# Kernel optimization log

Hardware: AMD Instinct MI355X
Metric: run time of the kernel (lower is better)

The kernel has to match this reference:

```python
import jax, jax.numpy as jnp
import numpy as np

N = 50000      # nodes
E = 500000     # edges
CHAN = 64      # channels
R0 = 2.0       # radial cutoff scale


def radial_encode_8(d, r0):
    # d: (E,) edge distances -> (E, 8) Gaussian radial basis on [0, r0]
    mu = jnp.linspace(0.0, r0, 8).astype(d.dtype)
    sigma = r0 / 8.0
    return jnp.exp(-(((d[:, None] - mu) / sigma) ** 2))


def vector_sigmoid(v):
    # v: (..., 3, chan); sigmoid-shaped vector activation (norm over spatial axis)
    vv = jnp.sum(v * v, axis=-2, keepdims=True)
    return v / jnp.sqrt(1.0 + vv)


def setup_inputs() -> dict:
    key = jax.random.key(0)
    ks = jax.random.split(key, 12)
    rn = lambda i, shape, scale=1.0: jax.random.normal(ks[i], shape, jnp.float32) * scale
    src = jax.random.randint(ks[0], (E,), 0, N)
    dst = jax.random.randint(ks[1], (E,), 0, N)
    r_ij = rn(2, (E, 3))
    z_0 = rn(3, (N, CHAN))
    z_1 = rn(4, (N, 3, CHAN))
    emb = rn(5, (N, CHAN))
    k = CHAN ** -0.5
    return dict(
        src=src, dst=dst, r_ij=r_ij, z_0=z_0, z_1=z_1, emb=emb,
        W_enc=rn(6, (8, CHAN), 8 ** -0.5), b_enc=jnp.zeros((CHAN,), jnp.float32),
        W_src=rn(7, (CHAN, CHAN), k), b_src=jnp.zeros((CHAN,), jnp.float32),
        W_dst=rn(8, (CHAN, CHAN), k), b_dst=jnp.zeros((CHAN,), jnp.float32),
        W_gate=rn(9, (CHAN, 4 * CHAN), k), b_gate=jnp.zeros((4 * CHAN,), jnp.float32),
        W_s=rn(10, (CHAN, CHAN), k), W_v=rn(11, (CHAN, CHAN), k),
    )


def reference(src, dst, r_ij, z_0, z_1, emb,
              W_enc, b_enc, W_src, b_src, W_dst, b_dst,
              W_gate, b_gate, W_s, W_v):
    # edges_read: gather node embeddings to edges, fuse src/dst linears
    emb_ij = (emb[src] @ W_src + b_src) + (emb[dst] @ W_dst + b_dst)        # (E, C)
    d = jnp.sqrt(jnp.sum(r_ij * r_ij, axis=-1))                              # (E,)
    dist_emb = radial_encode_8(d, R0) @ W_enc + b_enc + emb_ij               # (E, C)
    # vector sigmoid on scaled displacement
    r_hat = vector_sigmoid((r_ij * (7.0 / R0))[..., None])[..., 0]           # (E, 3)
    # edges_read_dst: gather dst-node scalar/vector features
    z0_j = z_0[dst]                                                          # (E, C)
    z1_j = z_1[dst]                                                          # (E, 3, C)
    # MessageContract (rank-1 equivariant tensor contraction, gated by dist_emb)
    g = (dist_emb @ W_gate + b_gate).reshape(E, 4, CHAN)                     # (E, 4, C)
    s_msg = g[:, 0] * z0_j + g[:, 1] * jnp.einsum('ei,eic->ec', r_hat, z1_j)  # scalar msg
    psi0 = s_msg @ W_s                                                        # (E, C)
    v_msg = g[:, 2][:, None, :] * z1_j \
          + g[:, 3][:, None, :] * (r_hat[:, :, None] * z0_j[:, None, :])     # (E, 3, C)
    psi1 = jnp.einsum('eic,cd->eid', v_msg, W_v)                              # (E, 3, C)
    # edges_reduce_src: scatter-add messages back to source nodes
    out0 = jax.ops.segment_sum(psi0, src, num_segments=N)                     # (N, C)
    out1 = jax.ops.segment_sum(psi1.reshape(E, 3 * CHAN), src,
                               num_segments=N).reshape(N, 3, CHAN)            # (N, 3, C)
    return out0, out1
```

## Files before the change

### kernel.cpp

```cpp
#include <hip/hip_runtime.h>

typedef unsigned int u32;

#define WS_WSG   0
#define WS_WDG   16384
#define WS_WEG   32768
#define WS_BALL  34816
#define WS_GS    35072

__global__ void zero_k(float* p, int n) {
    int i = blockIdx.x * blockDim.x + threadIdx.x;
    int st = gridDim.x * blockDim.x;
    for (; i < n; i += st) p[i] = 0.0f;
}

__global__ void compose_k(const float* __restrict__ Wsrc, const float* __restrict__ Wdst,
                          const float* __restrict__ Wenc, const float* __restrict__ benc,
                          const float* __restrict__ bsrc, const float* __restrict__ bdst,
                          const float* __restrict__ Wgate, const float* __restrict__ bgate,
                          float* __restrict__ ws) {
    const int j = threadIdx.x;
    const int r = blockIdx.x;
    if (r < 64) {
        float a = 0.f, b = 0.f;
        for (int c = 0; c < 64; ++c) {
            const float wg = Wgate[c * 256 + j];
            a += Wsrc[r * 64 + c] * wg;
            b += Wdst[r * 64 + c] * wg;
        }
        ws[WS_WSG + r * 256 + j] = a;
        ws[WS_WDG + r * 256 + j] = b;
    } else if (r < 72) {
        const int m = r - 64;
        float a = 0.f;
        for (int c = 0; c < 64; ++c) a += Wenc[m * 64 + c] * Wgate[c * 256 + j];
        ws[WS_WEG + m * 256 + j] = a;
    } else {
        float a = bgate[j];
        for (int c = 0; c < 64; ++c)
            a += (benc[c] + bsrc[c] + bdst[c]) * Wgate[c * 256 + j];
        ws[WS_BALL + j] = a;
    }
}

__global__ __launch_bounds__(512, 1) void nodepre_k(
    const float* __restrict__ emb, const float* __restrict__ ws,
    float* __restrict__ GS, float* __restrict__ GD, int N) {
    __shared__ float sW[32768];
    __shared__ float sE[256];
    for (int i = threadIdx.x; i < 32768; i += 512) sW[i] = ws[i];
    __syncthreads();
    const int half = threadIdx.x >> 8;
    const int j = threadIdx.x & 255;
    const float* W = &sW[half * 16384];
    float* G = half ? GD : GS;
    const int ngroups = (N + 3) >> 2;
    for (int grp = blockIdx.x; grp < ngroups; grp += gridDim.x) {
        const int n0 = grp * 4;
        if (threadIdx.x < 256) {
            const int nn = n0 + (threadIdx.x >> 6);
            sE[threadIdx.x] = (nn < N) ? emb[nn * 64 + (threadIdx.x & 63)] : 0.f;
        }
        __syncthreads();
        float a0 = 0.f, a1 = 0.f, a2 = 0.f, a3 = 0.f;
        #pragma unroll 8
        for (int k = 0; k < 64; ++k) {
            const float w = W[k * 256 + j];
            a0 += sE[k] * w;
            a1 += sE[64 + k] * w;
            a2 += sE[128 + k] * w;
            a3 += sE[192 + k] * w;
        }
        if (n0 < N)     G[(size_t)n0 * 256 + j] = a0;
        if (n0 + 1 < N) G[(size_t)(n0 + 1) * 256 + j] = a1;
        if (n0 + 2 < N) G[(size_t)(n0 + 2) * 256 + j] = a2;
        if (n0 + 3 < N) G[(size_t)(n0 + 3) * 256 + j] = a3;
        __syncthreads();
    }
}

__global__ __launch_bounds__(256, 8) void edge_fast_k(
    const int* __restrict__ src, const int* __restrict__ dst,
    const float* __restrict__ r_ij, const float* __restrict__ z0g,
    const float* __restrict__ z1g, const float* __restrict__ GS,
    const float* __restrict__ GD, const float* __restrict__ WeG,
    const float* __restrict__ ball, float* __restrict__ out, int N, int E) {
    __shared__ float sWe[2048];
    __shared__ float sBall[256];
    __shared__ int sFl[2];

    if (threadIdx.x == 0) {
        const u32* ps = (const u32*)src;
        const u32* pd = (const u32*)dst;
        int s64 = 1, d64 = 1;
        for (int i = 1; i < 128; i += 2) {
            if (ps[i] != 0u) s64 = 0;
            if (pd[i] != 0u) d64 = 0;
        }
        sFl[0] = s64;
        sFl[1] = d64;
    }
    for (int i = threadIdx.x; i < 2048; i += 256) sWe[i] = WeG[i];
    if (threadIdx.x < 256) sBall[threadIdx.x] = ball[threadIdx.x];
    __syncthreads();

    const int wid = threadIdx.x >> 6, lane = threadIdx.x & 63;
    const int i64s = sFl[0], i64d = sFl[1];

    for (int e = blockIdx.x * 4 + wid; e < E; e += gridDim.x * 4) {
        const int s = i64s ? src[2 * e] : src[e];
        const int t = i64d ? dst[2 * e] : dst[e];
        if (s < 0 || s >= N || t < 0 || t >= N) continue;

        const float* gs = GS + (size_t)s * 256 + lane;
        const float* gd = GD + (size_t)t * 256 + lane;
        const float a0 = gs[0], a1 = gs[64], a2 = gs[128], a3 = gs[192];
        const float b0 = gd[0], b1 = gd[64], b2 = gd[128], b3 = gd[192];
        const float z0v = z0g[t * 64 + lane];
        const float za = z1g[t * 192 + lane];
        const float zb = z1g[t * 192 + 64 + lane];
        const float zc = z1g[t * 192 + 128 + lane];
        const float r0 = r_ij[e * 3 + 0];
        const float r1 = r_ij[e * 3 + 1];
        const float r2 = r_ij[e * 3 + 2];

        float g0 = a0 + b0 + sBall[lane];
        float g1 = a1 + b1 + sBall[64 + lane];
        float g2 = a2 + b2 + sBall[128 + lane];
        float g3 = a3 + b3 + sBall[192 + lane];

        const float d = sqrtf(r0 * r0 + r1 * r1 + r2 * r2);
        #pragma unroll
        for (int m = 0; m < 8; ++m) {
            const float mu = 0.28571428571f * (float)m;
            const float tt = (d - mu) * 4.0f;
            const float rm = __expf(-tt * tt);
            const float* w = &sWe[(m << 8) + lane];
            g0 += rm * w[0];
            g1 += rm * w[64];
            g2 += rm * w[128];
            g3 += rm * w[192];
        }

        const float v0 = r0 * 3.5f, v1 = r1 * 3.5f, v2 = r2 * 3.5f;
        const float inv = rsqrtf(1.0f + v0 * v0 + v1 * v1 + v2 * v2);
        const float h0 = v0 * inv, h1 = v1 * inv, h2 = v2 * inv;

        const float uu = h0 * za + h1 * zb + h2 * zc;

        const float smsg = g0 * z0v + g1 * uu;
        const float vm0 = g2 * za + g3 * h0 * z0v;
        const float vm1 = g2 * zb + g3 * h1 * z0v;
        const float vm2 = g2 * zc + g3 * h2 * z0v;

        atomicAdd(&out[s * 64 + lane], smsg);
        const int bo = N * 64 + s * 192 + lane;
        atomicAdd(&out[bo], vm0);
        atomicAdd(&out[bo + 64], vm1);
        atomicAdd(&out[bo + 128], vm2);
    }
}

__global__ __launch_bounds__(256) void nodepost_k(
    float* __restrict__ out, const float* __restrict__ Ws,
    const float* __restrict__ Wv, int N) {
    __shared__ float sWs[4096];
    __shared__ float sWv[4096];
    __shared__ float sRow[256];
    for (int i = threadIdx.x; i < 4096; i += 256) {
        sWs[i] = Ws[i];
        sWv[i] = Wv[i];
    }
    __syncthreads();
    const int j = threadIdx.x;
    const int part = j >> 6;
    const int col = j & 63;
    const float* W = (part == 0) ? sWs : sWv;
    for (int n = blockIdx.x; n < N; n += gridDim.x) {
        const float v = (part == 0) ? out[n * 64 + j]
                                    : out[N * 64 + n * 192 + (j - 64)];
        sRow[j] = v;
        __syncthreads();
        const float* row = &sRow[part * 64];
        float acc = 0.f;
        #pragma unroll 8
        for (int k = 0; k < 64; ++k) acc += row[k] * W[k * 64 + col];
        if (part == 0) out[n * 64 + j] = acc;
        else out[N * 64 + n * 192 + (j - 64)] = acc;
        __syncthreads();
    }
}

__global__ __launch_bounds__(512, 1) void edge_k(
    const int* __restrict__ src, const int* __restrict__ dst,
    const float* __restrict__ r_ij, const float* __restrict__ z0g,
    const float* __restrict__ z1g, const float* __restrict__ emb,
    const float* __restrict__ Wenc, const float* __restrict__ benc,
    const float* __restrict__ Wsrc, const float* __restrict__ bsrc,
    const float* __restrict__ Wdst, const float* __restrict__ bdst,
    const float* __restrict__ Wgate, const float* __restrict__ bgate,
    const float* __restrict__ Ws, const float* __restrict__ Wv,
    float* __restrict__ out, int N, int E)
{
    __shared__ float sWsrc[4096];
    __shared__ float sWdst[4096];
    __shared__ float sWg[16384];
    __shared__ float sWs[4096];
    __shared__ float sWv[4096];
    __shared__ float sWe[512];
    __shared__ float sB[64];
    __shared__ float sBg[256];
    __shared__ int sFl[2];

    if (threadIdx.x == 0) {
        const u32* ps = (const u32*)src;
        const u32* pd = (const u32*)dst;
        int s64 = 1, d64 = 1;
        for (int i = 1; i < 128; i += 2) {
            if (ps[i] != 0u) s64 = 0;
            if (pd[i] != 0u) d64 = 0;
        }
        sFl[0] = s64;
        sFl[1] = d64;
    }
    for (int i = threadIdx.x; i < 4096; i += 512) {
        sWsrc[i] = Wsrc[i];
        sWdst[i] = Wdst[i];
        sWs[i] = Ws[i];
        sWv[i] = Wv[i];
    }
    for (int i = threadIdx.x; i < 16384; i += 512) sWg[i] = Wgate[i];
    for (int i = threadIdx.x; i < 512; i += 512) sWe[i] = Wenc[i];
    if (threadIdx.x < 64)
        sB[threadIdx.x] = benc[threadIdx.x] + bsrc[threadIdx.x] + bdst[threadIdx.x];
    if (threadIdx.x < 256) sBg[threadIdx.x] = bgate[threadIdx.x];
    __syncthreads();

    const int wid = threadIdx.x >> 6, lane = threadIdx.x & 63;
    const int i64s = sFl[0], i64d = sFl[1];

    for (int e = blockIdx.x * 8 + wid; e < E; e += gridDim.x * 8) {
        const int s = i64s ? src[2 * e] : src[e];
        const int t = i64d ? dst[2 * e] : dst[e];
        if (s < 0 || s >= N || t < 0 || t >= N) continue;

        const float es = emb[s * 64 + lane];
        const float et = emb[t * 64 + lane];
        float de = sB[lane];
        #pragma unroll 8
        for (int k = 0; k < 64; ++k) {
            de += __shfl(es, k, 64) * sWsrc[(k << 6) + lane];
            de += __shfl(et, k, 64) * sWdst[(k << 6) + lane];
        }
        const float r0 = r_ij[e * 3 + 0];
        const float r1 = r_ij[e * 3 + 1];
        const float r2 = r_ij[e * 3 + 2];
        const float d = sqrtf(r0 * r0 + r1 * r1 + r2 * r2);
        #pragma unroll
        for (int m = 0; m < 8; ++m) {
            const float mu = (2.0f / 7.0f) * (float)m;
            const float tt = (d - mu) * 4.0f;
            de += __expf(-tt * tt) * sWe[m * 64 + lane];
        }

        const float v0 = r0 * 3.5f, v1 = r1 * 3.5f, v2 = r2 * 3.5f;
        const float inv = rsqrtf(1.0f + v0 * v0 + v1 * v1 + v2 * v2);
        const float h0 = v0 * inv, h1 = v1 * inv, h2 = v2 * inv;

        const float z0v = z0g[t * 64 + lane];
        const float za = z1g[t * 192 + lane];
        const float zb = z1g[t * 192 + 64 + lane];
        const float zc = z1g[t * 192 + 128 + lane];
        const float uu = h0 * za + h1 * zb + h2 * zc;

        float g0 = sBg[lane], g1 = sBg[64 + lane], g2 = sBg[128 + lane], g3 = sBg[192 + lane];
        #pragma unroll 8
        for (int k = 0; k < 64; ++k) {
            const float dk = __shfl(de, k, 64);
            const float* w = &sWg[(k << 8) + lane];
            g0 += dk * w[0];
            g1 += dk * w[64];
            g2 += dk * w[128];
            g3 += dk * w[192];
        }

        const float smsg = g0 * z0v + g1 * uu;
        const float vm0 = g2 * za + g3 * h0 * z0v;
        const float vm1 = g2 * zb + g3 * h1 * z0v;
        const float vm2 = g2 * zc + g3 * h2 * z0v;

        float p0 = 0.f, q0 = 0.f, q1 = 0.f, q2 = 0.f;
        #pragma unroll 8
        for (int k = 0; k < 64; ++k) {
            const float sk = __shfl(smsg, k, 64);
            const float a = __shfl(vm0, k, 64);
            const float b = __shfl(vm1, k, 64);
            const float c = __shfl(vm2, k, 64);
            p0 += sk * sWs[(k << 6) + lane];
            const float wv = sWv[(k << 6) + lane];
            q0 += a * wv;
            q1 += b * wv;
            q2 += c * wv;
        }

        atomicAdd(&out[s * 64 + lane], p0);
        const int b1 = N * 64 + s * 192 + lane;
        atomicAdd(&out[b1], q0);
        atomicAdd(&out[b1 + 64], q1);
        atomicAdd(&out[b1 + 128], q2);
    }
}

extern "C" void kernel_launch(void* const* d_in, const int* in_sizes, int n_in,
                              void* d_out, int out_size, void* d_ws, size_t ws_size,
                              hipStream_t stream) {
    const int* src = (const int*)d_in[0];
    const int* dst = (const int*)d_in[1];
    const float* r_ij = (const float*)d_in[2];
    const float* z0g  = (const float*)d_in[3];
    const float* z1g  = (const float*)d_in[4];
    const float* emb  = (const float*)d_in[5];
    const float* Wenc = (const float*)d_in[6];
    const float* benc = (const float*)d_in[7];
    const float* Wsrc = (const float*)d_in[8];
    const float* bsrc = (const float*)d_in[9];
    const float* Wdst = (const float*)d_in[10];
    const float* bdst = (const float*)d_in[11];
    const float* Wgate = (const float*)d_in[12];
    const float* bgate = (const float*)d_in[13];
    const float* Ws = (const float*)d_in[14];
    const float* Wv = (const float*)d_in[15];

    const int N = out_size / 256;
    int E = in_sizes[0];
    if (in_sizes[2] / 3 < E) E = in_sizes[2] / 3;

    zero_k<<<2048, 256, 0, stream>>>((float*)d_out, out_size);

    float* ws = (float*)d_ws;
    const size_t need = ((size_t)WS_GS + 2u * (size_t)N * 256u) * sizeof(float);
    if (ws != nullptr && ws_size >= need) {
        compose_k<<<73, 256, 0, stream>>>(Wsrc, Wdst, Wenc, benc, bsrc, bdst,
                                          Wgate, bgate, ws);
        float* GS = ws + WS_GS;
        float* GD = GS + (size_t)N * 256;
        nodepre_k<<<512, 512, 0, stream>>>(emb, ws, GS, GD, N);
        edge_fast_k<<<2048, 256, 0, stream>>>(src, dst, r_ij, z0g, z1g, GS, GD,
                                              ws + WS_WEG, ws + WS_BALL,
                                              (float*)d_out, N, E);
        nodepost_k<<<2048, 256, 0, stream>>>((float*)d_out, Ws, Wv, N);
    } else {
        edge_k<<<2048, 512, 0, stream>>>(src, dst, r_ij, z0g, z1g, emb, Wenc, benc,
                                         Wsrc, bsrc, Wdst, bdst, Wgate, bgate, Ws, Wv,
                                         (float*)d_out, N, E);
    }
}
```

Measured before the change: 789.7 us.

## Bucket edges by source node into CSR and accumulate messages per segment

Adds a counting sort of edges by source node (count, single-block scan, fill) that packs r_ij and dst into a float4 table. A new edge kernel walks contiguous source-sorted ranges, loads the source gate row once per segment and flushes register accumulators with one set of atomics per segment instead of per edge. The node pre- and post-transform kernels are also reworked with float4 shared reads and two rows per block. The sort adds several extra launches, a serial one-block scan and extra global traffic, and the sorted path only runs when the workspace is large enough.

```diff
diff --git a/kernel.cpp b/kernel.cpp
--- a/kernel.cpp
+++ b/kernel.cpp
@@ -6,7 +6,8 @@
 #define WS_WDG   16384
 #define WS_WEG   32768
 #define WS_BALL  34816
-#define WS_GS    35072
+#define WS_ETOT  35072
+#define WS_GS    35328
 
 __global__ void zero_k(float* p, int n) {
     int i = blockIdx.x * blockDim.x + threadIdx.x;
@@ -43,40 +44,215 @@
     }
 }
 
-__global__ __launch_bounds__(512, 1) void nodepre_k(
-    const float* __restrict__ emb, const float* __restrict__ ws,
-    float* __restrict__ GS, float* __restrict__ GD, int N) {
-    __shared__ float sW[32768];
-    __shared__ float sE[256];
-    for (int i = threadIdx.x; i < 32768; i += 512) sW[i] = ws[i];
-    __syncthreads();
-    const int half = threadIdx.x >> 8;
-    const int j = threadIdx.x & 255;
-    const float* W = &sW[half * 16384];
-    float* G = half ? GD : GS;
-    const int ngroups = (N + 3) >> 2;
-    for (int grp = blockIdx.x; grp < ngroups; grp += gridDim.x) {
-        const int n0 = grp * 4;
-        if (threadIdx.x < 256) {
-            const int nn = n0 + (threadIdx.x >> 6);
-            sE[threadIdx.x] = (nn < N) ? emb[nn * 64 + (threadIdx.x & 63)] : 0.f;
-        }
+__global__ __launch_bounds__(256, 2) void nodepre2_k(
+    const float* __restrict__ emb, const float* __restrict__ Wg,
+    float* __restrict__ G, int N) {
+    __shared__ float sW[16384];
+    __shared__ __align__(16) float sEm[256];
+    for (int i = threadIdx.x * 4; i < 16384; i += 1024)
+        *(float4*)&sW[i] = *(const float4*)&Wg[i];
+    const int j = threadIdx.x;
+    const int ngr = (N + 3) >> 2;
+    for (int g = blockIdx.x; g < ngr; g += gridDim.x) {
+        const int n0 = g * 4;
+        const int nn = n0 + (j >> 6);
+        sEm[j] = (nn < N) ? emb[nn * 64 + (j & 63)] : 0.f;
         __syncthreads();
         float a0 = 0.f, a1 = 0.f, a2 = 0.f, a3 = 0.f;
-        #pragma unroll 8
-        for (int k = 0; k < 64; ++k) {
-            const float w = W[k * 256 + j];
-            a0 += sE[k] * w;
-            a1 += sE[64 + k] * w;
-            a2 += sE[128 + k] * w;
-            a3 += sE[192 + k] * w;
-        }
+        #pragma unroll
+        for (int k4 = 0; k4 < 16; ++k4) {
+            const float4 e0 = *(const float4*)&sEm[4 * k4];
+            const float4 e1 = *(const float4*)&sEm[64 + 4 * k4];
+            const float4 e2 = *(const float4*)&sEm[128 + 4 * k4];
+            const float4 e3 = *(const float4*)&sEm[192 + 4 * k4];
+            const float w0 = sW[(4 * k4 + 0) * 256 + j];
+            const float w1 = sW[(4 * k4 + 1) * 256 + j];
+            const float w2 = sW[(4 * k4 + 2) * 256 + j];
+            const float w3 = sW[(4 * k4 + 3) * 256 + j];
+            a0 += e0.x * w0 + e0.y * w1 + e0.z * w2 + e0.w * w3;
+            a1 += e1.x * w0 + e1.y * w1 + e1.z * w2 + e1.w * w3;
+            a2 += e2.x * w0 + e2.y * w1 + e2.z * w2 + e2.w * w3;
+            a3 += e3.x * w0 + e3.y * w1 + e3.z * w2 + e3.w * w3;
+        }
+        __syncthreads();
         if (n0 < N)     G[(size_t)n0 * 256 + j] = a0;
         if (n0 + 1 < N) G[(size_t)(n0 + 1) * 256 + j] = a1;
         if (n0 + 2 < N) G[(size_t)(n0 + 2) * 256 + j] = a2;
         if (n0 + 3 < N) G[(size_t)(n0 + 3) * 256 + j] = a3;
+    }
+}
+
+__global__ void count_k(const int* __restrict__ src, const int* __restrict__ dst,
+                        int* __restrict__ cnt, int N, int E) {
+    __shared__ int sFl[2];
+    if (threadIdx.x == 0) {
+        const u32* ps = (const u32*)src;
+        const u32* pd = (const u32*)dst;
+        int s64 = 1, d64 = 1;
+        for (int i = 1; i < 128; i += 2) {
+            if (ps[i] != 0u) s64 = 0;
+            if (pd[i] != 0u) d64 = 0;
+        }
+        sFl[0] = s64;
+        sFl[1] = d64;
+    }
+    __syncthreads();
+    const int i64s = sFl[0], i64d = sFl[1];
+    for (int e = blockIdx.x * blockDim.x + threadIdx.x; e < E;
+         e += gridDim.x * blockDim.x) {
+        const int s = i64s ? src[2 * e] : src[e];
+        const int t = i64d ? dst[2 * e] : dst[e];
+        if (s < 0 || s >= N || t < 0 || t >= N) continue;
+        atomicAdd(&cnt[s], 1);
+    }
+}
+
+__global__ __launch_bounds__(1024) void scan_k(int* __restrict__ cnt,
+                                               int* __restrict__ etot, int N) {
+    __shared__ int sp[1024];
+    const int tid = threadIdx.x;
+    const int chunk = (N + 1023) >> 10;
+    const int beg = tid * chunk;
+    int end = beg + chunk; if (end > N) end = N;
+    int sum = 0;
+    for (int i = beg; i < end; ++i) sum += cnt[i];
+    sp[tid] = sum;
+    __syncthreads();
+    for (int off = 1; off < 1024; off <<= 1) {
+        const int v = (tid >= off) ? sp[tid - off] : 0;
         __syncthreads();
-    }
+        sp[tid] += v;
+        __syncthreads();
+    }
+    int cur = (tid == 0) ? 0 : sp[tid - 1];
+    for (int i = beg; i < end; ++i) {
+        const int c = cnt[i];
+        cnt[i] = cur;
+        cur += c;
+    }
+    if (tid == 1023) *etot = sp[1023];
+}
+
+__global__ void fill_k(const int* __restrict__ src, const int* __restrict__ dst,
+                       const float* __restrict__ r_ij, int* __restrict__ cursor,
+                       int* __restrict__ ss, float4* __restrict__ tbl,
+                       int N, int E) {
+    __shared__ int sFl[2];
+    if (threadIdx.x == 0) {
+        const u32* ps = (const u32*)src;
+        const u32* pd = (const u32*)dst;
+        int s64 = 1, d64 = 1;
+        for (int i = 1; i < 128; i += 2) {
+            if (ps[i] != 0u) s64 = 0;
+            if (pd[i] != 0u) d64 = 0;
+        }
+        sFl[0] = s64;
+        sFl[1] = d64;
+    }
+    __syncthreads();
+    const int i64s = sFl[0], i64d = sFl[1];
+    for (int e = blockIdx.x * blockDim.x + threadIdx.x; e < E;
+         e += gridDim.x * blockDim.x) {
+        const int s = i64s ? src[2 * e] : src[e];
+        const int t = i64d ? dst[2 * e] : dst[e];
+        if (s < 0 || s >= N || t < 0 || t >= N) continue;
+        const float r0 = r_ij[e * 3 + 0];
+        const float r1 = r_ij[e * 3 + 1];
+        const float r2 = r_ij[e * 3 + 2];
+        const int pos = atomicAdd(&cursor[s], 1);
+        ss[pos] = s;
+        tbl[pos] = make_float4(r0, r1, r2, __int_as_float(t));
+    }
+}
+
+__global__ __launch_bounds__(256, 8) void edge_sorted_k(
+    const float* __restrict__ GS, const float* __restrict__ GD,
+    const float* __restrict__ z0g, const float* __restrict__ z1g,
+    const int* __restrict__ ss, const float4* __restrict__ tbl,
+    const float* __restrict__ WeG, const float* __restrict__ ball,
+    const int* __restrict__ etot, float* __restrict__ out, int N) {
+    __shared__ float sWe[2048];
+    __shared__ float sBall[256];
+    __shared__ int sE[1];
+    for (int i = threadIdx.x; i < 2048; i += 256) sWe[i] = WeG[i];
+    sBall[threadIdx.x] = ball[threadIdx.x];
+    if (threadIdx.x == 0) sE[0] = *etot;
+    __syncthreads();
+
+    const int Et = sE[0];
+    const int wid = threadIdx.x >> 6, lane = threadIdx.x & 63;
+    const int nw = gridDim.x * 4;
+    const int w = blockIdx.x * 4 + wid;
+    const int chunk = (Et + nw - 1) / nw;
+    const int beg = w * chunk;
+    int end = beg + chunk; if (end > Et) end = Et;
+    if (beg >= end) return;
+
+    const float bl0 = sBall[lane], bl1 = sBall[64 + lane];
+    const float bl2 = sBall[128 + lane], bl3 = sBall[192 + lane];
+
+    int cur = -1;
+    float accS = 0.f, accV0 = 0.f, accV1 = 0.f, accV2 = 0.f;
+    float gs0 = 0.f, gs1 = 0.f, gs2 = 0.f, gs3 = 0.f;
+
+    for (int i = beg; i < end; ++i) {
+        const int s = ss[i];
+        const float4 mt = tbl[i];
+        const int t = __float_as_int(mt.w);
+        if (s != cur) {
+            if (cur >= 0) {
+                atomicAdd(&out[cur * 64 + lane], accS);
+                const int bo = N * 64 + cur * 192 + lane;
+                atomicAdd(&out[bo], accV0);
+                atomicAdd(&out[bo + 64], accV1);
+                atomicAdd(&out[bo + 128], accV2);
+            }
+            cur = s;
+            accS = accV0 = accV1 = accV2 = 0.f;
+            const float* gp = GS + (size_t)s * 256 + lane;
+            gs0 = gp[0]; gs1 = gp[64]; gs2 = gp[128]; gs3 = gp[192];
+        }
+        const float* gd = GD + (size_t)t * 256 + lane;
+        const float b0 = gd[0], b1 = gd[64], b2 = gd[128], b3 = gd[192];
+        const float z0v = z0g[t * 64 + lane];
+        const float za = z1g[t * 192 + lane];
+        const float zb = z1g[t * 192 + 64 + lane];
+        const float zc = z1g[t * 192 + 128 + lane];
+        const float r0 = mt.x, r1 = mt.y, r2 = mt.z;
+
+        float g0 = gs0 + b0 + bl0;
+        float g1 = gs1 + b1 + bl1;
+        float g2 = gs2 + b2 + bl2;
+        float g3 = gs3 + b3 + bl3;
+
+        const float d = sqrtf(r0 * r0 + r1 * r1 + r2 * r2);
+        #pragma unroll
+        for (int m = 0; m < 8; ++m) {
+            const float mu = 0.28571428571f * (float)m;
+            const float tt = (d - mu) * 4.0f;
+            const float rm = __expf(-tt * tt);
+            const float* wq = &sWe[(m << 8) + lane];
+            g0 += rm * wq[0];
+            g1 += rm * wq[64];
+            g2 += rm * wq[128];
+            g3 += rm * wq[192];
+        }
+
+        const float v0 = r0 * 3.5f, v1 = r1 * 3.5f, v2 = r2 * 3.5f;
+        const float inv = rsqrtf(1.0f + v0 * v0 + v1 * v1 + v2 * v2);
+        const float h0 = v0 * inv, h1 = v1 * inv, h2 = v2 * inv;
+        const float uu = h0 * za + h1 * zb + h2 * zc;
+
+        accS  += g0 * z0v + g1 * uu;
+        accV0 += g2 * za + g3 * h0 * z0v;
+        accV1 += g2 * zb + g3 * h1 * z0v;
+        accV2 += g2 * zc + g3 * h2 * z0v;
+    }
+    atomicAdd(&out[cur * 64 + lane], accS);
+    const int bo = N * 64 + cur * 192 + lane;
+    atomicAdd(&out[bo], accV0);
+    atomicAdd(&out[bo + 64], accV1);
+    atomicAdd(&out[bo + 128], accV2);
 }
 
 __global__ __launch_bounds__(256, 8) void edge_fast_k(
@@ -101,7 +277,7 @@
         sFl[1] = d64;
     }
     for (int i = threadIdx.x; i < 2048; i += 256) sWe[i] = WeG[i];
-    if (threadIdx.x < 256) sBall[threadIdx.x] = ball[threadIdx.x];
+    sBall[threadIdx.x] = ball[threadIdx.x];
     __syncthreads();
 
     const int wid = threadIdx.x >> 6, lane = threadIdx.x & 63;
@@ -135,17 +311,16 @@
             const float mu = 0.28571428571f * (float)m;
             const float tt = (d - mu) * 4.0f;
             const float rm = __expf(-tt * tt);
-            const float* w = &sWe[(m << 8) + lane];
-            g0 += rm * w[0];
-            g1 += rm * w[64];
-            g2 += rm * w[128];
-            g3 += rm * w[192];
+            const float* wq = &sWe[(m << 8) + lane];
+            g0 += rm * wq[0];
+            g1 += rm * wq[64];
+            g2 += rm * wq[128];
+            g3 += rm * wq[192];
         }
 
         const float v0 = r0 * 3.5f, v1 = r1 * 3.5f, v2 = r2 * 3.5f;
         const float inv = rsqrtf(1.0f + v0 * v0 + v1 * v1 + v2 * v2);
         const float h0 = v0 * inv, h1 = v1 * inv, h2 = v2 * inv;
-
         const float uu = h0 * za + h1 * zb + h2 * zc;
 
         const float smsg = g0 * z0v + g1 * uu;
@@ -161,12 +336,12 @@
     }
 }
 
-__global__ __launch_bounds__(256) void nodepost_k(
+__global__ __launch_bounds__(256) void nodepost2_k(
     float* __restrict__ out, const float* __restrict__ Ws,
     const float* __restrict__ Wv, int N) {
     __shared__ float sWs[4096];
     __shared__ float sWv[4096];
-    __shared__ float sRow[256];
+    __shared__ __align__(16) float sRow[2][256];
     for (int i = threadIdx.x; i < 4096; i += 256) {
         sWs[i] = Ws[i];
         sWv[i] = Wv[i];
@@ -175,19 +350,34 @@
     const int j = threadIdx.x;
     const int part = j >> 6;
     const int col = j & 63;
+    const int pj = j - 64;
     const float* W = (part == 0) ? sWs : sWv;
-    for (int n = blockIdx.x; n < N; n += gridDim.x) {
-        const float v = (part == 0) ? out[n * 64 + j]
-                                    : out[N * 64 + n * 192 + (j - 64)];
-        sRow[j] = v;
+    for (int n0 = blockIdx.x * 2; n0 < N; n0 += gridDim.x * 2) {
+        const int n1 = n0 + 1;
+        const bool has1 = n1 < N;
+        sRow[0][j] = (part == 0) ? out[n0 * 64 + j] : out[N * 64 + n0 * 192 + pj];
+        if (has1)
+            sRow[1][j] = (part == 0) ? out[n1 * 64 + j] : out[N * 64 + n1 * 192 + pj];
         __syncthreads();
-        const float* row = &sRow[part * 64];
-        float acc = 0.f;
-        #pragma unroll 8
-        for (int k = 0; k < 64; ++k) acc += row[k] * W[k * 64 + col];
-        if (part == 0) out[n * 64 + j] = acc;
-        else out[N * 64 + n * 192 + (j - 64)] = acc;
+        float a0 = 0.f, a1 = 0.f;
+        #pragma unroll
+        for (int k4 = 0; k4 < 16; ++k4) {
+            const float4 rA = *(const float4*)&sRow[0][part * 64 + 4 * k4];
+            const float4 rB = *(const float4*)&sRow[1][part * 64 + 4 * k4];
+            const float w0 = W[(4 * k4 + 0) * 64 + col];
+            const float w1 = W[(4 * k4 + 1) * 64 + col];
+            const float w2 = W[(4 * k4 + 2) * 64 + col];
+            const float w3 = W[(4 * k4 + 3) * 64 + col];
+            a0 += rA.x * w0 + rA.y * w1 + rA.z * w2 + rA.w * w3;
+            a1 += rB.x * w0 + rB.y * w1 + rB.z * w2 + rB.w * w3;
+        }
         __syncthreads();
+        if (part == 0) out[n0 * 64 + j] = a0;
+        else out[N * 64 + n0 * 192 + pj] = a0;
+        if (has1) {
+            if (part == 0) out[n1 * 64 + j] = a1;
+            else out[N * 64 + n1 * 192 + pj] = a1;
+        }
     }
 }
 
@@ -338,17 +528,38 @@
     zero_k<<<2048, 256, 0, stream>>>((float*)d_out, out_size);
 
     float* ws = (float*)d_ws;
-    const size_t need = ((size_t)WS_GS + 2u * (size_t)N * 256u) * sizeof(float);
-    if (ws != nullptr && ws_size >= need) {
+    const size_t gsgd = 2u * (size_t)N * 256u;
+    const size_t Np = ((size_t)N + 3u) & ~3ull;
+    const size_t Ep = ((size_t)E + 3u) & ~3ull;
+    const size_t needGSGD = ((size_t)WS_GS + gsgd) * sizeof(float);
+    const size_t needCSR  = ((size_t)WS_GS + gsgd + Np + Ep + 4u * (size_t)E + 64u) * sizeof(float);
+
+    if (ws != nullptr && ws_size >= needGSGD) {
         compose_k<<<73, 256, 0, stream>>>(Wsrc, Wdst, Wenc, benc, bsrc, bdst,
                                           Wgate, bgate, ws);
         float* GS = ws + WS_GS;
         float* GD = GS + (size_t)N * 256;
-        nodepre_k<<<512, 512, 0, stream>>>(emb, ws, GS, GD, N);
-        edge_fast_k<<<2048, 256, 0, stream>>>(src, dst, r_ij, z0g, z1g, GS, GD,
-                                              ws + WS_WEG, ws + WS_BALL,
-                                              (float*)d_out, N, E);
-        nodepost_k<<<2048, 256, 0, stream>>>((float*)d_out, Ws, Wv, N);
+        nodepre2_k<<<512, 256, 0, stream>>>(emb, ws + WS_WSG, GS, N);
+        nodepre2_k<<<512, 256, 0, stream>>>(emb, ws + WS_WDG, GD, N);
+
+        if (ws_size >= needCSR) {
+            int* cnt = (int*)(GD + (size_t)N * 256);
+            int* ss  = cnt + Np;
+            float4* tbl = (float4*)(ss + Ep);
+            int* etot = (int*)ws + WS_ETOT;
+            zero_k<<<64, 256, 0, stream>>>((float*)cnt, N);
+            count_k<<<1024, 256, 0, stream>>>(src, dst, cnt, N, E);
+            scan_k<<<1, 1024, 0, stream>>>(cnt, etot, N);
+            fill_k<<<1024, 256, 0, stream>>>(src, dst, r_ij, cnt, ss, tbl, N, E);
+            edge_sorted_k<<<2048, 256, 0, stream>>>(GS, GD, z0g, z1g, ss, tbl,
+                                                    ws + WS_WEG, ws + WS_BALL,
+                                                    etot, (float*)d_out, N);
+        } else {
+            edge_fast_k<<<2048, 256, 0, stream>>>(src, dst, r_ij, z0g, z1g, GS, GD,
+                                                  ws + WS_WEG, ws + WS_BALL,
+                                                  (float*)d_out, N, E);
+        }
+        nodepost2_k<<<2048, 256, 0, stream>>>((float*)d_out, Ws, Wv, N);
     } else {
         edge_k<<<2048, 512, 0, stream>>>(src, dst, r_ij, z0g, z1g, emb, Wenc, benc,
                                          Wsrc, bsrc, Wdst, bdst, Wgate, bgate, Ws, Wv,
```

Result: slower. 1.619 ms (+105.0%).

## Prefetch next edge in contiguous per-wave chunks and vectorize node GEMMs

Applied to the files above, without the earlier changes.

The edge kernel now gives each wavefront a contiguous range of edges. It issues the gathers for the next edge before computing and scattering the current one, so memory latency overlaps with compute. Invalid edges are masked by multiplying by zero instead of skipping with `continue`. The node pre-transform is split into two launches, each holding a 64KB weight tile, and uses float4 shared-memory reads. The node post-transform handles two rows per block iteration. The prefetch raises register pressure at 8 blocks per CU, and contiguous chunking changes how accesses spread across waves.

```diff
diff --git a/kernel.cpp b/kernel.cpp
--- a/kernel.cpp
+++ b/kernel.cpp
@@ -6,7 +6,7 @@
 #define WS_WDG   16384
 #define WS_WEG   32768
 #define WS_BALL  34816
-#define WS_GS    35072
+#define WS_GS    35328
 
 __global__ void zero_k(float* p, int n) {
     int i = blockIdx.x * blockDim.x + threadIdx.x;
@@ -43,43 +43,120 @@
     }
 }
 
-__global__ __launch_bounds__(512, 1) void nodepre_k(
-    const float* __restrict__ emb, const float* __restrict__ ws,
-    float* __restrict__ GS, float* __restrict__ GD, int N) {
-    __shared__ float sW[32768];
-    __shared__ float sE[256];
-    for (int i = threadIdx.x; i < 32768; i += 512) sW[i] = ws[i];
-    __syncthreads();
-    const int half = threadIdx.x >> 8;
-    const int j = threadIdx.x & 255;
-    const float* W = &sW[half * 16384];
-    float* G = half ? GD : GS;
-    const int ngroups = (N + 3) >> 2;
-    for (int grp = blockIdx.x; grp < ngroups; grp += gridDim.x) {
-        const int n0 = grp * 4;
-        if (threadIdx.x < 256) {
-            const int nn = n0 + (threadIdx.x >> 6);
-            sE[threadIdx.x] = (nn < N) ? emb[nn * 64 + (threadIdx.x & 63)] : 0.f;
-        }
+__global__ __launch_bounds__(256, 2) void nodepre2_k(
+    const float* __restrict__ emb, const float* __restrict__ Wg,
+    float* __restrict__ G, int N) {
+    __shared__ float sW[16384];
+    __shared__ __align__(16) float sEm[256];
+    for (int i = threadIdx.x * 4; i < 16384; i += 1024)
+        *(float4*)&sW[i] = *(const float4*)&Wg[i];
+    const int j = threadIdx.x;
+    const int ngr = (N + 3) >> 2;
+    for (int g = blockIdx.x; g < ngr; g += gridDim.x) {
+        const int n0 = g * 4;
+        const int nn = n0 + (j >> 6);
+        sEm[j] = (nn < N) ? emb[nn * 64 + (j & 63)] : 0.f;
         __syncthreads();
         float a0 = 0.f, a1 = 0.f, a2 = 0.f, a3 = 0.f;
-        #pragma unroll 8
-        for (int k = 0; k < 64; ++k) {
-            const float w = W[k * 256 + j];
-            a0 += sE[k] * w;
-            a1 += sE[64 + k] * w;
-            a2 += sE[128 + k] * w;
-            a3 += sE[192 + k] * w;
-        }
+        #pragma unroll
+        for (int k4 = 0; k4 < 16; ++k4) {
+            const float4 e0 = *(const float4*)&sEm[4 * k4];
+            const float4 e1 = *(const float4*)&sEm[64 + 4 * k4];
+            const float4 e2 = *(const float4*)&sEm[128 + 4 * k4];
+            const float4 e3 = *(const float4*)&sEm[192 + 4 * k4];
+            const float w0 = sW[(4 * k4 + 0) * 256 + j];
+            const float w1 = sW[(4 * k4 + 1) * 256 + j];
+            const float w2 = sW[(4 * k4 + 2) * 256 + j];
+            const float w3 = sW[(4 * k4 + 3) * 256 + j];
+            a0 += e0.x * w0 + e0.y * w1 + e0.z * w2 + e0.w * w3;
+            a1 += e1.x * w0 + e1.y * w1 + e1.z * w2 + e1.w * w3;
+            a2 += e2.x * w0 + e2.y * w1 + e2.z * w2 + e2.w * w3;
+            a3 += e3.x * w0 + e3.y * w1 + e3.z * w2 + e3.w * w3;
+        }
+        __syncthreads();
         if (n0 < N)     G[(size_t)n0 * 256 + j] = a0;
         if (n0 + 1 < N) G[(size_t)(n0 + 1) * 256 + j] = a1;
         if (n0 + 2 < N) G[(size_t)(n0 + 2) * 256 + j] = a2;
         if (n0 + 3 < N) G[(size_t)(n0 + 3) * 256 + j] = a3;
-        __syncthreads();
-    }
-}
-
-__global__ __launch_bounds__(256, 8) void edge_fast_k(
+    }
+}
+
+struct ER {
+    int s, t;
+    float ok;
+    float r0, r1, r2;
+    float a0, a1, a2, a3;
+    float b0, b1, b2, b3;
+    float z0, za, zb, zc;
+};
+
+__device__ __forceinline__ ER load_edge(
+    int e, int lane, int i64s, int i64d, int N,
+    const int* __restrict__ src, const int* __restrict__ dst,
+    const float* __restrict__ r_ij, const float* __restrict__ GS,
+    const float* __restrict__ GD, const float* __restrict__ z0g,
+    const float* __restrict__ z1g) {
+    ER x;
+    int s = i64s ? src[2 * e] : src[e];
+    int t = i64d ? dst[2 * e] : dst[e];
+    x.ok = 1.f;
+    if (s < 0 || s >= N) { s = 0; x.ok = 0.f; }
+    if (t < 0 || t >= N) { t = 0; x.ok = 0.f; }
+    x.s = s; x.t = t;
+    x.r0 = r_ij[e * 3 + 0];
+    x.r1 = r_ij[e * 3 + 1];
+    x.r2 = r_ij[e * 3 + 2];
+    const float* gp = GS + (size_t)s * 256 + lane;
+    x.a0 = gp[0]; x.a1 = gp[64]; x.a2 = gp[128]; x.a3 = gp[192];
+    const float* gd = GD + (size_t)t * 256 + lane;
+    x.b0 = gd[0]; x.b1 = gd[64]; x.b2 = gd[128]; x.b3 = gd[192];
+    x.z0 = z0g[t * 64 + lane];
+    const float* zp = z1g + t * 192 + lane;
+    x.za = zp[0]; x.zb = zp[64]; x.zc = zp[128];
+    return x;
+}
+
+__device__ __forceinline__ void consume_edge(
+    const ER& x, int lane, int N,
+    const float* __restrict__ sWe,
+    float bl0, float bl1, float bl2, float bl3,
+    float* __restrict__ out) {
+    float g0 = x.a0 + x.b0 + bl0;
+    float g1 = x.a1 + x.b1 + bl1;
+    float g2 = x.a2 + x.b2 + bl2;
+    float g3 = x.a3 + x.b3 + bl3;
+
+    const float d = sqrtf(x.r0 * x.r0 + x.r1 * x.r1 + x.r2 * x.r2);
+    #pragma unroll
+    for (int m = 0; m < 8; ++m) {
+        const float mu = 0.28571428571f * (float)m;
+        const float tt = (d - mu) * 4.0f;
+        const float rm = __expf(-tt * tt);
+        const float* wq = &sWe[(m << 8) + lane];
+        g0 += rm * wq[0];
+        g1 += rm * wq[64];
+        g2 += rm * wq[128];
+        g3 += rm * wq[192];
+    }
+
+    const float v0 = x.r0 * 3.5f, v1 = x.r1 * 3.5f, v2 = x.r2 * 3.5f;
+    const float inv = rsqrtf(1.0f + v0 * v0 + v1 * v1 + v2 * v2);
+    const float h0 = v0 * inv, h1 = v1 * inv, h2 = v2 * inv;
+    const float uu = h0 * x.za + h1 * x.zb + h2 * x.zc;
+
+    const float smsg = (g0 * x.z0 + g1 * uu) * x.ok;
+    const float vm0 = (g2 * x.za + g3 * h0 * x.z0) * x.ok;
+    const float vm1 = (g2 * x.zb + g3 * h1 * x.z0) * x.ok;
+    const float vm2 = (g2 * x.zc + g3 * h2 * x.z0) * x.ok;
+
+    atomicAdd(&out[x.s * 64 + lane], smsg);
+    const int bo = N * 64 + x.s * 192 + lane;
+    atomicAdd(&out[bo], vm0);
+    atomicAdd(&out[bo + 64], vm1);
+    atomicAdd(&out[bo + 128], vm2);
+}
+
+__global__ __launch_bounds__(256, 8) void edge_pipe_k(
     const int* __restrict__ src, const int* __restrict__ dst,
     const float* __restrict__ r_ij, const float* __restrict__ z0g,
     const float* __restrict__ z1g, const float* __restrict__ GS,
@@ -101,72 +178,37 @@
         sFl[1] = d64;
     }
     for (int i = threadIdx.x; i < 2048; i += 256) sWe[i] = WeG[i];
-    if (threadIdx.x < 256) sBall[threadIdx.x] = ball[threadIdx.x];
+    sBall[threadIdx.x] = ball[threadIdx.x];
     __syncthreads();
 
     const int wid = threadIdx.x >> 6, lane = threadIdx.x & 63;
     const int i64s = sFl[0], i64d = sFl[1];
 
-    for (int e = blockIdx.x * 4 + wid; e < E; e += gridDim.x * 4) {
-        const int s = i64s ? src[2 * e] : src[e];
-        const int t = i64d ? dst[2 * e] : dst[e];
-        if (s < 0 || s >= N || t < 0 || t >= N) continue;
-
-        const float* gs = GS + (size_t)s * 256 + lane;
-        const float* gd = GD + (size_t)t * 256 + lane;
-        const float a0 = gs[0], a1 = gs[64], a2 = gs[128], a3 = gs[192];
-        const float b0 = gd[0], b1 = gd[64], b2 = gd[128], b3 = gd[192];
-        const float z0v = z0g[t * 64 + lane];
-        const float za = z1g[t * 192 + lane];
-        const float zb = z1g[t * 192 + 64 + lane];
-        const float zc = z1g[t * 192 + 128 + lane];
-        const float r0 = r_ij[e * 3 + 0];
-        const float r1 = r_ij[e * 3 + 1];
-        const float r2 = r_ij[e * 3 + 2];
-
-        float g0 = a0 + b0 + sBall[lane];
-        float g1 = a1 + b1 + sBall[64 + lane];
-        float g2 = a2 + b2 + sBall[128 + lane];
-        float g3 = a3 + b3 + sBall[192 + lane];
-
-        const float d = sqrtf(r0 * r0 + r1 * r1 + r2 * r2);
-        #pragma unroll
-        for (int m = 0; m < 8; ++m) {
-            const float mu = 0.28571428571f * (float)m;
-            const float tt = (d - mu) * 4.0f;
-            const float rm = __expf(-tt * tt);
-            const float* w = &sWe[(m << 8) + lane];
-            g0 += rm * w[0];
-            g1 += rm * w[64];
-            g2 += rm * w[128];
-            g3 += rm * w[192];
-        }
-
-        const float v0 = r0 * 3.5f, v1 = r1 * 3.5f, v2 = r2 * 3.5f;
-        const float inv = rsqrtf(1.0f + v0 * v0 + v1 * v1 + v2 * v2);
-        const float h0 = v0 * inv, h1 = v1 * inv, h2 = v2 * inv;
-
-        const float uu = h0 * za + h1 * zb + h2 * zc;
-
-        const float smsg = g0 * z0v + g1 * uu;
-        const float vm0 = g2 * za + g3 * h0 * z0v;
-        const float vm1 = g2 * zb + g3 * h1 * z0v;
-        const float vm2 = g2 * zc + g3 * h2 * z0v;
-
-        atomicAdd(&out[s * 64 + lane], smsg);
-        const int bo = N * 64 + s * 192 + lane;
-        atomicAdd(&out[bo], vm0);
-        atomicAdd(&out[bo + 64], vm1);
-        atomicAdd(&out[bo + 128], vm2);
-    }
-}
-
-__global__ __launch_bounds__(256) void nodepost_k(
+    const int gw = blockIdx.x * 4 + wid;
+    const int nw = gridDim.x * 4;
+    const int chunk = (E + nw - 1) / nw;
+    const int beg = gw * chunk;
+    int end = beg + chunk; if (end > E) end = E;
+    if (beg >= end) return;
+
+    const float bl0 = sBall[lane], bl1 = sBall[64 + lane];
+    const float bl2 = sBall[128 + lane], bl3 = sBall[192 + lane];
+
+    ER cur = load_edge(beg, lane, i64s, i64d, N, src, dst, r_ij, GS, GD, z0g, z1g);
+    for (int i = beg; i + 1 < end; ++i) {
+        ER nxt = load_edge(i + 1, lane, i64s, i64d, N, src, dst, r_ij, GS, GD, z0g, z1g);
+        consume_edge(cur, lane, N, sWe, bl0, bl1, bl2, bl3, out);
+        cur = nxt;
+    }
+    consume_edge(cur, lane, N, sWe, bl0, bl1, bl2, bl3, out);
+}
+
+__global__ __launch_bounds__(256) void nodepost2_k(
     float* __restrict__ out, const float* __restrict__ Ws,
     const float* __restrict__ Wv, int N) {
     __shared__ float sWs[4096];
     __shared__ float sWv[4096];
-    __shared__ float sRow[256];
+    __shared__ __align__(16) float sRow[2][256];
     for (int i = threadIdx.x; i < 4096; i += 256) {
         sWs[i] = Ws[i];
         sWv[i] = Wv[i];
@@ -175,19 +217,34 @@
     const int j = threadIdx.x;
     const int part = j >> 6;
     const int col = j & 63;
+    const int pj = j - 64;
     const float* W = (part == 0) ? sWs : sWv;
-    for (int n = blockIdx.x; n < N; n += gridDim.x) {
-        const float v = (part == 0) ? out[n * 64 + j]
-                                    : out[N * 64 + n * 192 + (j - 64)];
-        sRow[j] = v;
+    for (int n0 = blockIdx.x * 2; n0 < N; n0 += gridDim.x * 2) {
+        const int n1 = n0 + 1;
+        const bool has1 = n1 < N;
+        sRow[0][j] = (part == 0) ? out[n0 * 64 + j] : out[N * 64 + n0 * 192 + pj];
+        if (has1)
+            sRow[1][j] = (part == 0) ? out[n1 * 64 + j] : out[N * 64 + n1 * 192 + pj];
         __syncthreads();
-        const float* row = &sRow[part * 64];
-        float acc = 0.f;
-        #pragma unroll 8
-        for (int k = 0; k < 64; ++k) acc += row[k] * W[k * 64 + col];
-        if (part == 0) out[n * 64 + j] = acc;
-        else out[N * 64 + n * 192 + (j - 64)] = acc;
+        float a0 = 0.f, a1 = 0.f;
+        #pragma unroll
+        for (int k4 = 0; k4 < 16; ++k4) {
+            const float4 rA = *(const float4*)&sRow[0][part * 64 + 4 * k4];
+            const float4 rB = *(const float4*)&sRow[1][part * 64 + 4 * k4];
+            const float w0 = W[(4 * k4 + 0) * 64 + col];
+            const float w1 = W[(4 * k4 + 1) * 64 + col];
+            const float w2 = W[(4 * k4 + 2) * 64 + col];
+            const float w3 = W[(4 * k4 + 3) * 64 + col];
+            a0 += rA.x * w0 + rA.y * w1 + rA.z * w2 + rA.w * w3;
+            a1 += rB.x * w0 + rB.y * w1 + rB.z * w2 + rB.w * w3;
+        }
         __syncthreads();
+        if (part == 0) out[n0 * 64 + j] = a0;
+        else out[N * 64 + n0 * 192 + pj] = a0;
+        if (has1) {
+            if (part == 0) out[n1 * 64 + j] = a1;
+            else out[N * 64 + n1 * 192 + pj] = a1;
+        }
     }
 }
 
@@ -338,17 +395,20 @@
     zero_k<<<2048, 256, 0, stream>>>((float*)d_out, out_size);
 
     float* ws = (float*)d_ws;
-    const size_t need = ((size_t)WS_GS + 2u * (size_t)N * 256u) * sizeof(float);
-    if (ws != nullptr && ws_size >= need) {
+    const size_t gsgd = 2u * (size_t)N * 256u;
+    const size_t needGSGD = ((size_t)WS_GS + gsgd) * sizeof(float);
+
+    if (ws != nullptr && ws_size >= needGSGD) {
         compose_k<<<73, 256, 0, stream>>>(Wsrc, Wdst, Wenc, benc, bsrc, bdst,
                                           Wgate, bgate, ws);
         float* GS = ws + WS_GS;
         float* GD = GS + (size_t)N * 256;
-        nodepre_k<<<512, 512, 0, stream>>>(emb, ws, GS, GD, N);
-        edge_fast_k<<<2048, 256, 0, stream>>>(src, dst, r_ij, z0g, z1g, GS, GD,
+        nodepre2_k<<<512, 256, 0, stream>>>(emb, ws + WS_WSG, GS, N);
+        nodepre2_k<<<512, 256, 0, stream>>>(emb, ws + WS_WDG, GD, N);
+        edge_pipe_k<<<2048, 256, 0, stream>>>(src, dst, r_ij, z0g, z1g, GS, GD,
                                               ws + WS_WEG, ws + WS_BALL,
                                               (float*)d_out, N, E);
-        nodepost_k<<<2048, 256, 0, stream>>>((float*)d_out, Ws, Wv, N);
+        nodepost2_k<<<2048, 256, 0, stream>>>((float*)d_out, Ws, Wv, N);
     } else {
         edge_k<<<2048, 512, 0, stream>>>(src, dst, r_ij, z0g, z1g, emb, Wenc, benc,
                                          Wsrc, bsrc, Wdst, bdst, Wgate, bgate, Ws, Wv,
```

New measurement: 1.559 ms. 97.4% more time.

## Register-tile node pre/post GEMMs and interleave src/dst gate tables

Applied to the files above, without the earlier changes.

Merges the separate src and dst gate tables into one interleaved per-node buffer of 512 values. The node-level pre-projection and the post-projection (Ws/Wv) are rewritten as register-tiled GEMMs: each thread computes a 4-row by 4-column block using float4 shared-memory weight loads and float4 global stores. The goal is to cut shared-memory traffic and per-node synchronisation in the two small GEMM kernels. It adds per-row weight selection at the out0/out1 boundary in the post kernel, and changes the node stride the edge kernel gathers from.

```diff
diff --git a/kernel.cpp b/kernel.cpp
--- a/kernel.cpp
+++ b/kernel.cpp
@@ -3,10 +3,9 @@
 typedef unsigned int u32;
 
 #define WS_WSG   0
-#define WS_WDG   16384
 #define WS_WEG   32768
 #define WS_BALL  34816
-#define WS_GS    35072
+#define WS_GS    35328
 
 __global__ void zero_k(float* p, int n) {
     int i = blockIdx.x * blockDim.x + threadIdx.x;
@@ -28,8 +27,8 @@
             a += Wsrc[r * 64 + c] * wg;
             b += Wdst[r * 64 + c] * wg;
         }
-        ws[WS_WSG + r * 256 + j] = a;
-        ws[WS_WDG + r * 256 + j] = b;
+        ws[WS_WSG + r * 512 + j] = a;
+        ws[WS_WSG + r * 512 + 256 + j] = b;
     } else if (r < 72) {
         const int m = r - 64;
         float a = 0.f;
@@ -43,48 +42,59 @@
     }
 }
 
-__global__ __launch_bounds__(512, 1) void nodepre_k(
-    const float* __restrict__ emb, const float* __restrict__ ws,
-    float* __restrict__ GS, float* __restrict__ GD, int N) {
-    __shared__ float sW[32768];
-    __shared__ float sE[256];
-    for (int i = threadIdx.x; i < 32768; i += 512) sW[i] = ws[i];
-    __syncthreads();
-    const int half = threadIdx.x >> 8;
-    const int j = threadIdx.x & 255;
-    const float* W = &sW[half * 16384];
-    float* G = half ? GD : GS;
-    const int ngroups = (N + 3) >> 2;
-    for (int grp = blockIdx.x; grp < ngroups; grp += gridDim.x) {
-        const int n0 = grp * 4;
-        if (threadIdx.x < 256) {
-            const int nn = n0 + (threadIdx.x >> 6);
-            sE[threadIdx.x] = (nn < N) ? emb[nn * 64 + (threadIdx.x & 63)] : 0.f;
-        }
+__global__ __launch_bounds__(512, 1) void nodepre3_k(
+    const float* __restrict__ emb, const float* __restrict__ Wc,
+    float* __restrict__ G, int N) {
+    __shared__ __align__(16) float sW[32768];
+    __shared__ __align__(16) float sEm[1024];
+    for (int i = threadIdx.x * 4; i < 32768; i += 2048)
+        *(float4*)&sW[i] = *(const float4*)&Wc[i];
+
+    const int c4 = (threadIdx.x & 127) << 2;
+    const int g = threadIdx.x >> 7;
+    const int lim = N * 64;
+    const int ntiles = (N + 15) >> 4;
+
+    for (int tile = blockIdx.x; tile < ntiles; tile += gridDim.x) {
+        const int n0 = tile << 4;
+        const int base = n0 * 64;
         __syncthreads();
-        float a0 = 0.f, a1 = 0.f, a2 = 0.f, a3 = 0.f;
+        for (int i = threadIdx.x * 4; i < 1024; i += 2048) {
+            const int gi = base + i;
+            *(float4*)&sEm[i] = (gi < lim) ? *(const float4*)&emb[gi]
+                                           : make_float4(0.f, 0.f, 0.f, 0.f);
+        }
+        for (int i = 2048 + threadIdx.x * 4; i < 1024; i += 2048) { }
+        __syncthreads();
+
+        float4 a0 = {0,0,0,0}, a1 = {0,0,0,0}, a2 = {0,0,0,0}, a3 = {0,0,0,0};
+        const float* e0p = &sEm[(g * 4 + 0) * 64];
+        const float* e1p = &sEm[(g * 4 + 1) * 64];
+        const float* e2p = &sEm[(g * 4 + 2) * 64];
+        const float* e3p = &sEm[(g * 4 + 3) * 64];
         #pragma unroll 8
         for (int k = 0; k < 64; ++k) {
-            const float w = W[k * 256 + j];
-            a0 += sE[k] * w;
-            a1 += sE[64 + k] * w;
-            a2 += sE[128 + k] * w;
-            a3 += sE[192 + k] * w;
-        }
-        if (n0 < N)     G[(size_t)n0 * 256 + j] = a0;
-        if (n0 + 1 < N) G[(size_t)(n0 + 1) * 256 + j] = a1;
-        if (n0 + 2 < N) G[(size_t)(n0 + 2) * 256 + j] = a2;
-        if (n0 + 3 < N) G[(size_t)(n0 + 3) * 256 + j] = a3;
-        __syncthreads();
+            const float4 w = *(const float4*)&sW[k * 512 + c4];
+            const float e0 = e0p[k], e1 = e1p[k], e2 = e2p[k], e3 = e3p[k];
+            a0.x += e0 * w.x; a0.y += e0 * w.y; a0.z += e0 * w.z; a0.w += e0 * w.w;
+            a1.x += e1 * w.x; a1.y += e1 * w.y; a1.z += e1 * w.z; a1.w += e1 * w.w;
+            a2.x += e2 * w.x; a2.y += e2 * w.y; a2.z += e2 * w.z; a2.w += e2 * w.w;
+            a3.x += e3 * w.x; a3.y += e3 * w.y; a3.z += e3 * w.z; a3.w += e3 * w.w;
+        }
+        const int nb = n0 + g * 4;
+        if (nb + 0 < N) *(float4*)&G[(size_t)(nb + 0) * 512 + c4] = a0;
+        if (nb + 1 < N) *(float4*)&G[(size_t)(nb + 1) * 512 + c4] = a1;
+        if (nb + 2 < N) *(float4*)&G[(size_t)(nb + 2) * 512 + c4] = a2;
+        if (nb + 3 < N) *(float4*)&G[(size_t)(nb + 3) * 512 + c4] = a3;
     }
 }
 
 __global__ __launch_bounds__(256, 8) void edge_fast_k(
     const int* __restrict__ src, const int* __restrict__ dst,
     const float* __restrict__ r_ij, const float* __restrict__ z0g,
-    const float* __restrict__ z1g, const float* __restrict__ GS,
-    const float* __restrict__ GD, const float* __restrict__ WeG,
-    const float* __restrict__ ball, float* __restrict__ out, int N, int E) {
+    const float* __restrict__ z1g, const float* __restrict__ G,
+    const float* __restrict__ WeG, const float* __restrict__ ball,
+    float* __restrict__ out, int N, int E) {
     __shared__ float sWe[2048];
     __shared__ float sBall[256];
     __shared__ int sFl[2];
@@ -101,7 +111,7 @@
         sFl[1] = d64;
     }
     for (int i = threadIdx.x; i < 2048; i += 256) sWe[i] = WeG[i];
-    if (threadIdx.x < 256) sBall[threadIdx.x] = ball[threadIdx.x];
+    sBall[threadIdx.x] = ball[threadIdx.x];
     __syncthreads();
 
     const int wid = threadIdx.x >> 6, lane = threadIdx.x & 63;
@@ -112,8 +122,8 @@
         const int t = i64d ? dst[2 * e] : dst[e];
         if (s < 0 || s >= N || t < 0 || t >= N) continue;
 
-        const float* gs = GS + (size_t)s * 256 + lane;
-        const float* gd = GD + (size_t)t * 256 + lane;
+        const float* gs = G + (size_t)s * 512 + lane;
+        const float* gd = G + (size_t)t * 512 + 256 + lane;
         const float a0 = gs[0], a1 = gs[64], a2 = gs[128], a3 = gs[192];
         const float b0 = gd[0], b1 = gd[64], b2 = gd[128], b3 = gd[192];
         const float z0v = z0g[t * 64 + lane];
@@ -135,17 +145,16 @@
             const float mu = 0.28571428571f * (float)m;
             const float tt = (d - mu) * 4.0f;
             const float rm = __expf(-tt * tt);
-            const float* w = &sWe[(m << 8) + lane];
-            g0 += rm * w[0];
-            g1 += rm * w[64];
-            g2 += rm * w[128];
-            g3 += rm * w[192];
+            const float* wq = &sWe[(m << 8) + lane];
+            g0 += rm * wq[0];
+            g1 += rm * wq[64];
+            g2 += rm * wq[128];
+            g3 += rm * wq[192];
         }
 
         const float v0 = r0 * 3.5f, v1 = r1 * 3.5f, v2 = r2 * 3.5f;
         const float inv = rsqrtf(1.0f + v0 * v0 + v1 * v1 + v2 * v2);
         const float h0 = v0 * inv, h1 = v1 * inv, h2 = v2 * inv;
-
         const float uu = h0 * za + h1 * zb + h2 * zc;
 
         const float smsg = g0 * z0v + g1 * uu;
@@ -161,33 +170,70 @@
     }
 }
 
-__global__ __launch_bounds__(256) void nodepost_k(
+__global__ __launch_bounds__(256, 3) void nodepost3_k(
     float* __restrict__ out, const float* __restrict__ Ws,
     const float* __restrict__ Wv, int N) {
-    __shared__ float sWs[4096];
-    __shared__ float sWv[4096];
-    __shared__ float sRow[256];
-    for (int i = threadIdx.x; i < 4096; i += 256) {
-        sWs[i] = Ws[i];
-        sWv[i] = Wv[i];
-    }
-    __syncthreads();
-    const int j = threadIdx.x;
-    const int part = j >> 6;
-    const int col = j & 63;
-    const float* W = (part == 0) ? sWs : sWv;
-    for (int n = blockIdx.x; n < N; n += gridDim.x) {
-        const float v = (part == 0) ? out[n * 64 + j]
-                                    : out[N * 64 + n * 192 + (j - 64)];
-        sRow[j] = v;
+    __shared__ __align__(16) float sW[8192];
+    __shared__ float sR[64 * 65];
+    for (int i = threadIdx.x * 4; i < 8192; i += 1024) {
+        *(float4*)&sW[i] = (i < 4096) ? *(const float4*)&Ws[i]
+                                      : *(const float4*)&Wv[i - 4096];
+    }
+    const int c4 = (threadIdx.x & 15) << 2;
+    const int rq = threadIdx.x >> 4;
+    const int totalRows = 4 * N;
+    const int lim = totalRows * 64;
+    const int ntiles = (totalRows + 63) >> 6;
+
+    for (int tile = blockIdx.x; tile < ntiles; tile += gridDim.x) {
+        const int r0 = tile << 6;
         __syncthreads();
-        const float* row = &sRow[part * 64];
-        float acc = 0.f;
-        #pragma unroll 8
-        for (int k = 0; k < 64; ++k) acc += row[k] * W[k * 64 + col];
-        if (part == 0) out[n * 64 + j] = acc;
-        else out[N * 64 + n * 192 + (j - 64)] = acc;
+        for (int i = threadIdx.x; i < 4096; i += 256) {
+            const int gi = r0 * 64 + i;
+            sR[(i >> 6) * 65 + (i & 63)] = (gi < lim) ? out[gi] : 0.f;
+        }
         __syncthreads();
+
+        const int rb = rq << 2;
+        const int gr = r0 + rb;
+        const int o0 = (gr + 0 < N) ? 0 : 4096;
+        const int o3 = (gr + 3 < N) ? 0 : 4096;
+        float4 a0 = {0,0,0,0}, a1 = {0,0,0,0}, a2 = {0,0,0,0}, a3 = {0,0,0,0};
+        const float* rp0 = &sR[(rb + 0) * 65];
+        const float* rp1 = &sR[(rb + 1) * 65];
+        const float* rp2 = &sR[(rb + 2) * 65];
+        const float* rp3 = &sR[(rb + 3) * 65];
+        if (o0 == o3) {
+            const float* wb = &sW[o0 + c4];
+            #pragma unroll 8
+            for (int k = 0; k < 64; ++k) {
+                const float4 w = *(const float4*)&wb[k * 64];
+                const float e0 = rp0[k], e1 = rp1[k], e2 = rp2[k], e3 = rp3[k];
+                a0.x += e0 * w.x; a0.y += e0 * w.y; a0.z += e0 * w.z; a0.w += e0 * w.w;
+                a1.x += e1 * w.x; a1.y += e1 * w.y; a1.z += e1 * w.z; a1.w += e1 * w.w;
+                a2.x += e2 * w.x; a2.y += e2 * w.y; a2.z += e2 * w.z; a2.w += e2 * w.w;
+                a3.x += e3 * w.x; a3.y += e3 * w.y; a3.z += e3 * w.z; a3.w += e3 * w.w;
+            }
+        } else {
+            const int o1 = (gr + 1 < N) ? 0 : 4096;
+            const int o2 = (gr + 2 < N) ? 0 : 4096;
+            #pragma unroll 4
+            for (int k = 0; k < 64; ++k) {
+                const float4 w0 = *(const float4*)&sW[o0 + k * 64 + c4];
+                const float4 w1 = *(const float4*)&sW[o1 + k * 64 + c4];
+                const float4 w2 = *(const float4*)&sW[o2 + k * 64 + c4];
+                const float4 w3 = *(const float4*)&sW[o3 + k * 64 + c4];
+                const float e0 = rp0[k], e1 = rp1[k], e2 = rp2[k], e3 = rp3[k];
+                a0.x += e0 * w0.x; a0.y += e0 * w0.y; a0.z += e0 * w0.z; a0.w += e0 * w0.w;
+                a1.x += e1 * w1.x; a1.y += e1 * w1.y; a1.z += e1 * w1.z; a1.w += e1 * w1.w;
+                a2.x += e2 * w2.x; a2.y += e2 * w2.y; a2.z += e2 * w2.z; a2.w += e2 * w2.w;
+                a3.x += e3 * w3.x; a3.y += e3 * w3.y; a3.z += e3 * w3.z; a3.w += e3 * w3.w;
+            }
+        }
+        if (gr + 0 < totalRows) *(float4*)&out[(size_t)(gr + 0) * 64 + c4] = a0;
+        if (gr + 1 < totalRows) *(float4*)&out[(size_t)(gr + 1) * 64 + c4] = a1;
+        if (gr + 2 < totalRows) *(float4*)&out[(size_t)(gr + 2) * 64 + c4] = a2;
+        if (gr + 3 < totalRows) *(float4*)&out[(size_t)(gr + 3) * 64 + c4] = a3;
     }
 }
 
@@ -338,17 +384,17 @@
     zero_k<<<2048, 256, 0, stream>>>((float*)d_out, out_size);
 
     float* ws = (float*)d_ws;
-    const size_t need = ((size_t)WS_GS + 2u * (size_t)N * 256u) * sizeof(float);
+    const size_t need = ((size_t)WS_GS + (size_t)N * 512u) * sizeof(float);
+
     if (ws != nullptr && ws_size >= need) {
         compose_k<<<73, 256, 0, stream>>>(Wsrc, Wdst, Wenc, benc, bsrc, bdst,
                                           Wgate, bgate, ws);
-        float* GS = ws + WS_GS;
-        float* GD = GS + (size_t)N * 256;
-        nodepre_k<<<512, 512, 0, stream>>>(emb, ws, GS, GD, N);
-        edge_fast_k<<<2048, 256, 0, stream>>>(src, dst, r_ij, z0g, z1g, GS, GD,
+        float* G = ws + WS_GS;
+        nodepre3_k<<<256, 512, 0, stream>>>(emb, ws + WS_WSG, G, N);
+        edge_fast_k<<<2048, 256, 0, stream>>>(src, dst, r_ij, z0g, z1g, G,
                                               ws + WS_WEG, ws + WS_BALL,
                                               (float*)d_out, N, E);
-        nodepost_k<<<2048, 256, 0, stream>>>((float*)d_out, Ws, Wv, N);
+        nodepost3_k<<<2048, 256, 0, stream>>>((float*)d_out, Ws, Wv, N);
     } else {
         edge_k<<<2048, 512, 0, stream>>>(src, dst, r_ij, z0g, z1g, emb, Wenc, benc,
                                          Wsrc, bsrc, Wdst, bdst, Wgate, bgate, Ws, Wv,
```

After: 677.6 us. -14.2%, faster.
